# Kernel tuning notes

Measured on AMD Instinct MI355X. Metric: run time of the kernel, lower is better.

The kernel has to match this reference:

```python
import jax, jax.numpy as jnp
from jax import lax
import numpy as np

# Finite stand-in for torch's -inf mask value; avoids inf/nan issues under AD
# while leaving the argmax-based selection identical (kernel entries are O(1)).
NEG_MASK = -1e30


def cdpruner_select(image_features, last_layer_attention_avg_image, topk):
    """Greedy DPP (fast-MAP) token selection; faithful port of cdpruner().
    image_features: (B, N, D); last_layer_attention_avg_image: (B, N).
    Returns selected indices for batch 0, shape (topk,).
    """
    B, N, D = image_features.shape
    xn = image_features / jnp.linalg.norm(image_features, axis=-1, keepdims=True)
    xn = xn.astype(jnp.float32)
    similarity = jnp.einsum('bnd,bmd->bnm', xn, xn)          # (B, N, N)
    rel = -last_layer_attention_avg_image.astype(jnp.float32)
    rel = (rel - rel.min() + 1e-6) / (rel.max() - rel.min())  # global min/max, like torch .min()/.max()
    kernel = rel[:, :, None] * similarity * rel[:, None, :]   # (B, N, N)

    di2s0 = jnp.diagonal(kernel, axis1=1, axis2=2)            # (B, N)
    cis0 = jnp.zeros((topk, B, N), jnp.float32)
    bar = jnp.arange(B)

    def step(carry, i):
        cis, di2s = carry
        j = jnp.argmax(di2s, axis=-1)                         # (B,)
        kj = kernel[bar, j]                                   # (B, N)
        cis_j = cis[:, bar, j]                                # (topk, B); rows >= i are zero
        proj = jnp.einsum('tb,tbn->bn', cis_j, cis)           # == sum over first i rows
        eis = (kj - proj) / jnp.sqrt(di2s[bar, j])[:, None]   # (B, N)
        cis = cis.at[i].set(eis)
        di2s = di2s - jnp.square(eis)
        di2s = di2s.at[bar, j].set(NEG_MASK)
        return (cis, di2s), j

    _, js = lax.scan(step, (cis0, di2s0), jnp.arange(topk))   # js: (topk, B)
    return js[:, 0]                                           # select_idx.t()[0]


def setup_inputs() -> dict:
    key = jax.random.key(0)
    k1, k2 = jax.random.split(key)
    B, N, D = 1, 4096, 1024
    return {
        'image_features': jax.random.normal(k1, (B, N, D), jnp.float32),
        'last_layer_attention_avg_image': jax.random.uniform(k2, (B, N), jnp.float32),
        'topk_image_token_num': 128,
    }


def reference(image_features, last_layer_attention_avg_image, topk_image_token_num):
    sel = cdpruner_select(image_features, last_layer_attention_avg_image,
                          topk_image_token_num)
    # Downstream the model gathers the kept tokens; return the pruned features
    # (float output, shape (topk, D)) so fwd and fwd+bwd references agree.
    return image_features[0, sel]
```

## Files before the change

### kernel.cpp

```cpp
#include <hip/hip_runtime.h>
#include <hip/hip_bf16.h>
#include <stdint.h>

#define NTOK 4096
#define DIM  1024
#define TOPK 128
#define GB   32
#define GT   128
#define NEGM -1e30f

typedef __attribute__((ext_vector_type(8))) short bf16x8;
typedef __attribute__((ext_vector_type(4))) float f32x4;

__global__ __launch_bounds__(1024) void k_prep(const float* __restrict__ attn,
                                               float* __restrict__ rel) {
  __shared__ float smx[16], smn[16];
  int tid = threadIdx.x;
  float mx = -3.4e38f, mn = 3.4e38f;
  for (int n = tid; n < NTOK; n += 1024) {
    float a = attn[n];
    mx = fmaxf(mx, a); mn = fminf(mn, a);
  }
  for (int o = 32; o >= 1; o >>= 1) {
    mx = fmaxf(mx, __shfl_down(mx, o, 64));
    mn = fminf(mn, __shfl_down(mn, o, 64));
  }
  if ((tid & 63) == 0) { smx[tid >> 6] = mx; smn[tid >> 6] = mn; }
  __syncthreads();
  if (tid == 0) {
    float MX = smx[0], MN = smn[0];
    for (int w = 1; w < 16; ++w) { MX = fmaxf(MX, smx[w]); MN = fminf(MN, smn[w]); }
    smx[0] = MX; smn[0] = MN;
  }
  __syncthreads();
  float amax = smx[0], amin = smn[0];
  float rmin  = -amax;
  float range = (-amin) - rmin;
  for (int n = tid; n < NTOK; n += 1024) {
    float r = -attn[n];
    rel[n] = ((r - rmin) + 1e-6f) / range;
  }
}

__global__ __launch_bounds__(256) void k_norm(const float* __restrict__ x,
                                              __hip_bfloat16* __restrict__ H,
                                              __hip_bfloat16* __restrict__ L) {
  __shared__ float ps[4];
  int row = blockIdx.x, tid = threadIdx.x;
  const float4* xr = (const float4*)(x + (size_t)row * DIM);
  float4 v = xr[tid];
  float s = v.x * v.x + v.y * v.y + v.z * v.z + v.w * v.w;
  for (int o = 32; o >= 1; o >>= 1) s += __shfl_down(s, o, 64);
  if ((tid & 63) == 0) ps[tid >> 6] = s;
  __syncthreads();
  if (tid == 0) ps[0] = ps[0] + ps[1] + ps[2] + ps[3];
  __syncthreads();
  float nrm = sqrtf(ps[0]);
  float xf[4] = {v.x / nrm, v.y / nrm, v.z / nrm, v.w / nrm};
  __hip_bfloat16 hh[4], ll[4];
#pragma unroll
  for (int e = 0; e < 4; ++e) {
    hh[e] = __float2bfloat16(xf[e]);
    float lof = xf[e] - __bfloat162float(hh[e]);
    ll[e] = __float2bfloat16(lof);
  }
  *(short4*)(H + (size_t)row * DIM + tid * 4) = *(short4*)hh;
  *(short4*)(L + (size_t)row * DIM + tid * 4) = *(short4*)ll;
}

#define GBK 64
__global__ __launch_bounds__(256) void k_gemm(const __hip_bfloat16* __restrict__ H,
                                              const __hip_bfloat16* __restrict__ L,
                                              const float* __restrict__ rel,
                                              float* __restrict__ ker) {
  int bi = blockIdx.y, bj = blockIdx.x;
  if (bi > bj) return;
  __shared__ __align__(16) char smem[36864];
  int tid = threadIdx.x;
  int lane = tid & 63, wid = tid >> 6;
  int wr = wid >> 1, wc = wid & 1;
  int lm = lane & 15, quad = lane >> 4;
  const __hip_bfloat16* PA[4] = {H, H, L, L};
  const __hip_bfloat16* PB[4] = {H, L, H, L};
  int srow = wid * 32 + (lane >> 3);
  int kcs  = (lane & 7) ^ ((lane >> 3) & 7);
  f32x4 acc[4][4];
#pragma unroll
  for (int r = 0; r < 4; ++r)
#pragma unroll
    for (int c = 0; c < 4; ++c) acc[r][c] = (f32x4){0.f, 0.f, 0.f, 0.f};

  for (int kt = 0; kt < 4096; kt += GBK) {
    int p = kt >> 10, kk = kt & 1023;
    const __hip_bfloat16* Ab = PA[p] + (size_t)(bi * 128) * DIM + kk;
    const __hip_bfloat16* Bb = PB[p] + (size_t)(bj * 128) * DIM + kk;
    __syncthreads();
#pragma unroll
    for (int q = 0; q < 4; ++q) {
      const __hip_bfloat16* ga = Ab + (size_t)(srow + q * 8) * DIM + kcs * 8;
      const __hip_bfloat16* gb = Bb + (size_t)(srow + q * 8) * DIM + kcs * 8;
      __builtin_amdgcn_global_load_lds(
          (const __attribute__((address_space(1))) void*)ga,
          (__attribute__((address_space(3))) void*)(smem + (wid * 4 + q) * 1024),
          16, 0, 0);
      __builtin_amdgcn_global_load_lds(
          (const __attribute__((address_space(1))) void*)gb,
          (__attribute__((address_space(3))) void*)(smem + 16384 +
                                                    (wid * 4 + q) * 1024),
          16, 0, 0);
    }
    __syncthreads();
#pragma unroll
    for (int kq = 0; kq < 2; ++kq) {
      int kc = kq * 4 + quad;
      bf16x8 af[4], bff[4];
#pragma unroll
      for (int r = 0; r < 4; ++r) {
        int row = wr * 64 + r * 16 + lm;
        af[r] = *(const bf16x8*)(smem + row * 128 + ((kc ^ (lm & 7)) * 16));
      }
#pragma unroll
      for (int c = 0; c < 4; ++c) {
        int row = wc * 64 + c * 16 + lm;
        bff[c] = *(const bf16x8*)(smem + 16384 + row * 128 +
                                  ((kc ^ (lm & 7)) * 16));
      }
#pragma unroll
      for (int r = 0; r < 4; ++r)
#pragma unroll
        for (int c = 0; c < 4; ++c)
          acc[r][c] = __builtin_amdgcn_mfma_f32_16x16x32_bf16(
              af[r], bff[c], acc[r][c], 0, 0, 0);
    }
  }
  float rr[16], rc[4];
#pragma unroll
  for (int r = 0; r < 4; ++r)
#pragma unroll
    for (int e = 0; e < 4; ++e)
      rr[r * 4 + e] = rel[bi * 128 + wr * 64 + r * 16 + quad * 4 + e];
#pragma unroll
  for (int c = 0; c < 4; ++c) rc[c] = rel[bj * 128 + wc * 64 + c * 16 + lm];
#pragma unroll
  for (int r = 0; r < 4; ++r) {
    int grow = bi * 128 + wr * 64 + r * 16 + quad * 4;
#pragma unroll
    for (int c = 0; c < 4; ++c) {
      int gcol = bj * 128 + wc * 64 + c * 16 + lm;
#pragma unroll
      for (int e = 0; e < 4; ++e)
        ker[(size_t)(grow + e) * NTOK + gcol] =
            (acc[r][c][e] * rr[r * 4 + e]) * rc[c];
    }
  }
  if (bi != bj) {
    __syncthreads();
    float* Tw = (float*)(smem + wid * 4672);
#pragma unroll
    for (int c = 0; c < 4; ++c) {
#pragma unroll
      for (int r = 0; r < 4; ++r)
#pragma unroll
        for (int e = 0; e < 4; ++e)
          Tw[lm * 73 + r * 16 + quad * 4 + e] =
              (acc[r][c][e] * rc[c]) * rr[r * 4 + e];
      __syncthreads();
      int cc2 = lane >> 2, seg = lane & 3;
      float* dst = &ker[(size_t)(bj * 128 + wc * 64 + c * 16 + cc2) * NTOK +
                        bi * 128 + wr * 64 + seg * 16];
#pragma unroll
      for (int e = 0; e < 4; ++e)
        *(float4*)&dst[e * 4] = *(const float4*)&Tw[cc2 * 73 + seg * 16 + e * 4];
      __syncthreads();
    }
  }
}

__global__ __launch_bounds__(GT) void k_greedy(const float* __restrict__ ker,
                                               const float* __restrict__ feat,
                                               float* __restrict__ out,
                                               float* __restrict__ cisT,
                                               unsigned long long* __restrict__ slots) {
  __shared__ __align__(16) float histT[GT][132];
  __shared__ __align__(16) float colbuf[TOPK];
  __shared__ unsigned long long redw[GT / 64];
  __shared__ unsigned long long bwS;
  __shared__ int selj[TOPK];
  int tid = threadIdx.x;
  int lane = tid & 63, wid = tid >> 6;
  int blk = blockIdx.x;
  int n = blk * GT + tid;
  float di2s = ker[(size_t)n * NTOK + n];
#pragma unroll
  for (int t = 0; t < TOPK; t += 4)
    *(float4*)&histT[tid][t] = (float4){0.f, 0.f, 0.f, 0.f};

  for (int i = 0; i < TOPK; ++i) {
    unsigned u = __float_as_uint(di2s);
    unsigned key = (u & 0x80000000u) ? ~u : (u | 0x80000000u);
    unsigned long long pk =
        ((unsigned long long)key << 32) | (unsigned)(NTOK - 1 - n);
    for (int o = 32; o >= 1; o >>= 1) {
      unsigned long long q = __shfl_down(pk, o, 64);
      if (q > pk) pk = q;
    }
    if (lane == 0) redw[wid] = pk;
    __syncthreads();
    if (tid == 0) {
      unsigned long long m = redw[0];
      if (redw[1] > m) m = redw[1];
      __hip_atomic_store(&slots[((size_t)i * GB + blk) * 8], m,
                         __ATOMIC_RELEASE, __HIP_MEMORY_SCOPE_AGENT);
    }
    if (wid == 0) {
      unsigned long long v = 0;
      if (lane < GB) {
        do {
          v = __hip_atomic_load(&slots[((size_t)i * GB + lane) * 8],
                                __ATOMIC_RELAXED, __HIP_MEMORY_SCOPE_AGENT);
        } while (v == 0);
      }
      unsigned long long b1 = v;
      for (int o = 32; o >= 1; o >>= 1) {
        unsigned long long q = __shfl_down(b1, o, 64);
        if (q > b1) b1 = q;
      }
      b1 = __shfl(b1, 0, 64);
      __builtin_amdgcn_fence(__ATOMIC_ACQUIRE, "agent");
      int jw = NTOK - 1 - (int)(b1 & 0xffffffffu);
      unsigned long long cu = __hip_atomic_load(
          (const unsigned long long*)(cisT + (size_t)jw * TOPK) + lane,
          __ATOMIC_RELAXED, __HIP_MEMORY_SCOPE_AGENT);
      union { unsigned long long u64; float f[2]; } cc; cc.u64 = cu;
      colbuf[lane * 2]     = cc.f[0];
      colbuf[lane * 2 + 1] = cc.f[1];
      if (lane == 0) bwS = b1;
    }
    __syncthreads();
    unsigned long long b1 = bwS;
    int j = NTOK - 1 - (int)(b1 & 0xffffffffu);
    unsigned kw = (unsigned)(b1 >> 32);
    unsigned du = (kw & 0x80000000u) ? (kw & 0x7fffffffu) : ~kw;
    float sd = sqrtf(__uint_as_float(du));
    if (tid == 0) selj[i] = j;
    float kj = ker[(size_t)j * NTOK + n];
    float proj = 0.f;
    for (int t = 0; t < i; t += 4) {
      float4 c4 = *(const float4*)&colbuf[t];
      float4 h4 = *(const float4*)&histT[tid][t];
      proj += c4.x * h4.x + c4.y * h4.y + c4.z * h4.z + c4.w * h4.w;
    }
    float eis = (kj - proj) / sd;
    __hip_atomic_store(&cisT[(size_t)n * TOPK + i], eis, __ATOMIC_RELAXED,
                       __HIP_MEMORY_SCOPE_AGENT);
    histT[tid][i] = eis;
    di2s -= eis * eis;
    if (n == j) di2s = NEGM;
  }
  __syncthreads();
  for (int k = blk; k < TOPK; k += GB) {
    int j = selj[k];
    const float4* src = (const float4*)(feat + (size_t)j * DIM);
    float4* dst = (float4*)(out + (size_t)k * DIM);
    dst[tid]       = src[tid];
    dst[tid + GT]  = src[tid + GT];
  }
}

extern "C" void kernel_launch(void* const* d_in, const int* in_sizes, int n_in,
                              void* d_out, int out_size, void* d_ws, size_t ws_size,
                              hipStream_t stream) {
  const float* feat = (const float*)d_in[0];
  const float* attn = (const float*)d_in[1];
  float* out = (float*)d_out;
  char* ws = (char*)d_ws;

  unsigned long long* slots = (unsigned long long*)ws;
  float* rel = (float*)(ws + 262144);
  __hip_bfloat16* H = (__hip_bfloat16*)(ws + (1 << 20));
  __hip_bfloat16* L = (__hip_bfloat16*)(ws + (1 << 20) + (8 << 20));
  float* cisT = (float*)(ws + (1 << 20) + (16 << 20));
  float* ker  = (float*)(ws + (1 << 20) + (16 << 20) + (4 << 20));

  hipMemsetAsync(d_ws, 0, 262144, stream);
  k_prep<<<1, 1024, 0, stream>>>(attn, rel);
  k_norm<<<NTOK, 256, 0, stream>>>(feat, H, L);
  k_gemm<<<dim3(32, 32), 256, 0, stream>>>(H, L, rel, ker);
  k_greedy<<<GB, GT, 0, stream>>>(ker, feat, out, cisT, slots);
}
```

Measured before the change: 638.2 us.

## Use single-wavefront greedy blocks across 64 blocks to drop intra-block barriers

The greedy DPP kernel now runs 64 blocks of one 64-lane wavefront each, instead of 32 blocks of two wavefronts. Each block's argmax is a single wave shuffle reduction, and every lane polls one block's slot and reduces across the grid itself. This removes the shared-memory handoff and one of the two __syncthreads per iteration. The trade-off is twice as many blocks writing and polling slots, so the slots region and its memset are doubled.

```diff
diff --git a/kernel.cpp b/kernel.cpp
--- a/kernel.cpp
+++ b/kernel.cpp
@@ -5,8 +5,8 @@
 #define NTOK 4096
 #define DIM  1024
 #define TOPK 128
-#define GB   32
-#define GT   128
+#define GB   64
+#define GT   64
 #define NEGM -1e30f
 
 typedef __attribute__((ext_vector_type(8))) short bf16x8;
@@ -183,11 +183,8 @@
                                                unsigned long long* __restrict__ slots) {
   __shared__ __align__(16) float histT[GT][132];
   __shared__ __align__(16) float colbuf[TOPK];
-  __shared__ unsigned long long redw[GT / 64];
-  __shared__ unsigned long long bwS;
   __shared__ int selj[TOPK];
   int tid = threadIdx.x;
-  int lane = tid & 63, wid = tid >> 6;
   int blk = blockIdx.x;
   int n = blk * GT + tid;
   float di2s = ker[(size_t)n * NTOK + n];
@@ -204,46 +201,34 @@
       unsigned long long q = __shfl_down(pk, o, 64);
       if (q > pk) pk = q;
     }
-    if (lane == 0) redw[wid] = pk;
-    __syncthreads();
-    if (tid == 0) {
-      unsigned long long m = redw[0];
-      if (redw[1] > m) m = redw[1];
-      __hip_atomic_store(&slots[((size_t)i * GB + blk) * 8], m,
+    if (tid == 0)
+      __hip_atomic_store(&slots[((size_t)i * GB + blk) * 8], pk,
                          __ATOMIC_RELEASE, __HIP_MEMORY_SCOPE_AGENT);
-    }
-    if (wid == 0) {
-      unsigned long long v = 0;
-      if (lane < GB) {
-        do {
-          v = __hip_atomic_load(&slots[((size_t)i * GB + lane) * 8],
-                                __ATOMIC_RELAXED, __HIP_MEMORY_SCOPE_AGENT);
-        } while (v == 0);
-      }
-      unsigned long long b1 = v;
-      for (int o = 32; o >= 1; o >>= 1) {
-        unsigned long long q = __shfl_down(b1, o, 64);
-        if (q > b1) b1 = q;
-      }
-      b1 = __shfl(b1, 0, 64);
-      __builtin_amdgcn_fence(__ATOMIC_ACQUIRE, "agent");
-      int jw = NTOK - 1 - (int)(b1 & 0xffffffffu);
-      unsigned long long cu = __hip_atomic_load(
-          (const unsigned long long*)(cisT + (size_t)jw * TOPK) + lane,
-          __ATOMIC_RELAXED, __HIP_MEMORY_SCOPE_AGENT);
-      union { unsigned long long u64; float f[2]; } cc; cc.u64 = cu;
-      colbuf[lane * 2]     = cc.f[0];
-      colbuf[lane * 2 + 1] = cc.f[1];
-      if (lane == 0) bwS = b1;
-    }
-    __syncthreads();
-    unsigned long long b1 = bwS;
+    unsigned long long v;
+    do {
+      v = __hip_atomic_load(&slots[((size_t)i * GB + tid) * 8],
+                            __ATOMIC_RELAXED, __HIP_MEMORY_SCOPE_AGENT);
+    } while (v == 0);
+    unsigned long long b1 = v;
+    for (int o = 32; o >= 1; o >>= 1) {
+      unsigned long long q = __shfl_down(b1, o, 64);
+      if (q > b1) b1 = q;
+    }
+    b1 = __shfl(b1, 0, 64);
+    __builtin_amdgcn_fence(__ATOMIC_ACQUIRE, "agent");
     int j = NTOK - 1 - (int)(b1 & 0xffffffffu);
     unsigned kw = (unsigned)(b1 >> 32);
     unsigned du = (kw & 0x80000000u) ? (kw & 0x7fffffffu) : ~kw;
     float sd = sqrtf(__uint_as_float(du));
     if (tid == 0) selj[i] = j;
+    unsigned long long cu = __hip_atomic_load(
+        (const unsigned long long*)(cisT + (size_t)j * TOPK) + tid,
+        __ATOMIC_RELAXED, __HIP_MEMORY_SCOPE_AGENT);
     float kj = ker[(size_t)j * NTOK + n];
+    union { unsigned long long u64; float f[2]; } cc; cc.u64 = cu;
+    colbuf[tid * 2]     = cc.f[0];
+    colbuf[tid * 2 + 1] = cc.f[1];
+    __syncthreads();
     float proj = 0.f;
     for (int t = 0; t < i; t += 4) {
       float4 c4 = *(const float4*)&colbuf[t];
@@ -262,8 +247,8 @@
     int j = selj[k];
     const float4* src = (const float4*)(feat + (size_t)j * DIM);
     float4* dst = (float4*)(out + (size_t)k * DIM);
-    dst[tid]       = src[tid];
-    dst[tid + GT]  = src[tid + GT];
+#pragma unroll
+    for (int e = 0; e < 4; ++e) dst[tid + e * GT] = src[tid + e * GT];
   }
 }
 
@@ -276,13 +261,13 @@
   char* ws = (char*)d_ws;
 
   unsigned long long* slots = (unsigned long long*)ws;
-  float* rel = (float*)(ws + 262144);
+  float* rel = (float*)(ws + 524288);
   __hip_bfloat16* H = (__hip_bfloat16*)(ws + (1 << 20));
   __hip_bfloat16* L = (__hip_bfloat16*)(ws + (1 << 20) + (8 << 20));
   float* cisT = (float*)(ws + (1 << 20) + (16 << 20));
   float* ker  = (float*)(ws + (1 << 20) + (16 << 20) + (4 << 20));
 
-  hipMemsetAsync(d_ws, 0, 262144, stream);
+  hipMemsetAsync(d_ws, 0, 524288, stream);
   k_prep<<<1, 1024, 0, stream>>>(attn, rel);
   k_norm<<<NTOK, 256, 0, stream>>>(feat, H, L);
   k_gemm<<<dim3(32, 32), 256, 0, stream>>>(H, L, rel, ker);
```

Measured after the change: 679.9 us. 1.07x slower.

## Double-buffer GEMM LDS tiles and load hi/lo splits together per k-step

Applied to the files above, without the earlier changes.

Reworks the split-bf16 similarity GEMM to double-buffer its LDS tiles. The next k-slice is prefetched via global_load_lds while MFMAs run on the current buffer, so each step needs one barrier instead of two. Each stage now loads H and L tiles for both A and B at the same k offset and issues four MFMAs per fragment pair. This reuses A/B fragments across the hi/lo products instead of streaming the four products sequentially over 4096 k. LDS use rises to 64KB per block, which may reduce occupancy.

```diff
diff --git a/kernel.cpp b/kernel.cpp
--- a/kernel.cpp
+++ b/kernel.cpp
@@ -68,71 +68,85 @@
   *(short4*)(L + (size_t)row * DIM + tid * 4) = *(short4*)ll;
 }
 
-#define GBK 64
 __global__ __launch_bounds__(256) void k_gemm(const __hip_bfloat16* __restrict__ H,
                                               const __hip_bfloat16* __restrict__ L,
                                               const float* __restrict__ rel,
                                               float* __restrict__ ker) {
   int bi = blockIdx.y, bj = blockIdx.x;
   if (bi > bj) return;
-  __shared__ __align__(16) char smem[36864];
+  __shared__ __align__(16) char smem[65536];
   int tid = threadIdx.x;
   int lane = tid & 63, wid = tid >> 6;
   int wr = wid >> 1, wc = wid & 1;
   int lm = lane & 15, quad = lane >> 4;
-  const __hip_bfloat16* PA[4] = {H, H, L, L};
-  const __hip_bfloat16* PB[4] = {H, L, H, L};
-  int srow = wid * 32 + (lane >> 3);
-  int kcs  = (lane & 7) ^ ((lane >> 3) & 7);
+  int lrow = lane >> 2;
+  int kcf  = (lane & 3) ^ ((lane >> 2) & 3);
+  const __hip_bfloat16* M[4] = {
+      H + (size_t)(bi * 128) * DIM, L + (size_t)(bi * 128) * DIM,
+      H + (size_t)(bj * 128) * DIM, L + (size_t)(bj * 128) * DIM};
   f32x4 acc[4][4];
 #pragma unroll
   for (int r = 0; r < 4; ++r)
 #pragma unroll
     for (int c = 0; c < 4; ++c) acc[r][c] = (f32x4){0.f, 0.f, 0.f, 0.f};
 
-  for (int kt = 0; kt < 4096; kt += GBK) {
-    int p = kt >> 10, kk = kt & 1023;
-    const __hip_bfloat16* Ab = PA[p] + (size_t)(bi * 128) * DIM + kk;
-    const __hip_bfloat16* Bb = PB[p] + (size_t)(bj * 128) * DIM + kk;
+#define ISSUE_STAGE(s, pbuf)                                                   \
+  {                                                                            \
+    int kk = (s) * 32;                                                         \
+    char* base = smem + (pbuf) * 32768;                                        \
+    _Pragma("unroll")                                                          \
+    for (int m = 0; m < 4; ++m) {                                              \
+      _Pragma("unroll")                                                        \
+      for (int q = 0; q < 2; ++q) {                                            \
+        int r0 = wid * 32 + q * 16;                                            \
+        const __hip_bfloat16* g =                                              \
+            M[m] + (size_t)(r0 + lrow) * DIM + kk + kcf * 8;                   \
+        __builtin_amdgcn_global_load_lds(                                      \
+            (const __attribute__((address_space(1))) void*)g,                  \
+            (__attribute__((address_space(3))) void*)(base + m * 8192 +        \
+                                                      r0 * 64),                \
+            16, 0, 0);                                                         \
+      }                                                                        \
+    }                                                                          \
+  }
+
+  ISSUE_STAGE(0, 0);
+  int p = 0;
+  for (int s = 0; s < 32; ++s) {
     __syncthreads();
-#pragma unroll
-    for (int q = 0; q < 4; ++q) {
-      const __hip_bfloat16* ga = Ab + (size_t)(srow + q * 8) * DIM + kcs * 8;
-      const __hip_bfloat16* gb = Bb + (size_t)(srow + q * 8) * DIM + kcs * 8;
-      __builtin_amdgcn_global_load_lds(
-          (const __attribute__((address_space(1))) void*)ga,
-          (__attribute__((address_space(3))) void*)(smem + (wid * 4 + q) * 1024),
-          16, 0, 0);
-      __builtin_amdgcn_global_load_lds(
-          (const __attribute__((address_space(1))) void*)gb,
-          (__attribute__((address_space(3))) void*)(smem + 16384 +
-                                                    (wid * 4 + q) * 1024),
-          16, 0, 0);
-    }
-    __syncthreads();
-#pragma unroll
-    for (int kq = 0; kq < 2; ++kq) {
-      int kc = kq * 4 + quad;
-      bf16x8 af[4], bff[4];
-#pragma unroll
-      for (int r = 0; r < 4; ++r) {
-        int row = wr * 64 + r * 16 + lm;
-        af[r] = *(const bf16x8*)(smem + row * 128 + ((kc ^ (lm & 7)) * 16));
+    if (s + 1 < 32) ISSUE_STAGE(s + 1, 1 - p);
+    const char* b = smem + p * 32768;
+    bf16x8 aH[4], aL[4], bH[4], bL[4];
+#pragma unroll
+    for (int r = 0; r < 4; ++r) {
+      int row = wr * 64 + r * 16 + lm;
+      int off = row * 64 + ((quad ^ (lm & 3)) * 16);
+      aH[r] = *(const bf16x8*)(b + off);
+      aL[r] = *(const bf16x8*)(b + 8192 + off);
+    }
+#pragma unroll
+    for (int c = 0; c < 4; ++c) {
+      int row = wc * 64 + c * 16 + lm;
+      int off = row * 64 + ((quad ^ (lm & 3)) * 16);
+      bH[c] = *(const bf16x8*)(b + 16384 + off);
+      bL[c] = *(const bf16x8*)(b + 24576 + off);
+    }
+#pragma unroll
+    for (int r = 0; r < 4; ++r)
+#pragma unroll
+      for (int c = 0; c < 4; ++c) {
+        acc[r][c] = __builtin_amdgcn_mfma_f32_16x16x32_bf16(aH[r], bH[c],
+                                                            acc[r][c], 0, 0, 0);
+        acc[r][c] = __builtin_amdgcn_mfma_f32_16x16x32_bf16(aH[r], bL[c],
+                                                            acc[r][c], 0, 0, 0);
+        acc[r][c] = __builtin_amdgcn_mfma_f32_16x16x32_bf16(aL[r], bH[c],
+                                                            acc[r][c], 0, 0, 0);
+        acc[r][c] = __builtin_amdgcn_mfma_f32_16x16x32_bf16(aL[r], bL[c],
+                                                            acc[r][c], 0, 0, 0);
       }
-#pragma unroll
-      for (int c = 0; c < 4; ++c) {
-        int row = wc * 64 + c * 16 + lm;
-        bff[c] = *(const bf16x8*)(smem + 16384 + row * 128 +
-                                  ((kc ^ (lm & 7)) * 16));
-      }
-#pragma unroll
-      for (int r = 0; r < 4; ++r)
-#pragma unroll
-        for (int c = 0; c < 4; ++c)
-          acc[r][c] = __builtin_amdgcn_mfma_f32_16x16x32_bf16(
-              af[r], bff[c], acc[r][c], 0, 0, 0);
-    }
-  }
+    p ^= 1;
+  }
+#undef ISSUE_STAGE
   float rr[16], rc[4];
 #pragma unroll
   for (int r = 0; r < 4; ++r)
```

Result: faster. 572.0 us (-10.4%).
